# Optimization experiments

Hardware: AMD Instinct MI355X
Metric: run time of the kernel (lower is better)

The kernel has to match this reference:

```python
import jax, jax.numpy as jnp
import numpy as np

B, C, T = 64, 512, 4096
R = 8
H = C // R  # bottleneck = 64


def setup_inputs() -> dict:
    key = jax.random.key(0)
    k1, k2, k3, k4, k5 = jax.random.split(key, 5)
    x = jax.random.normal(k1, (B, C, T), dtype=jnp.float32)
    # PyTorch Linear default init: U(-1/sqrt(fan_in), 1/sqrt(fan_in))
    s1 = 1.0 / np.sqrt(C)
    s2 = 1.0 / np.sqrt(H)
    W1 = jax.random.uniform(k2, (H, C), dtype=jnp.float32, minval=-s1, maxval=s1)
    b1 = jax.random.uniform(k3, (H,), dtype=jnp.float32, minval=-s1, maxval=s1)
    W2 = jax.random.uniform(k4, (C, H), dtype=jnp.float32, minval=-s2, maxval=s2)
    b2 = jax.random.uniform(k5, (C,), dtype=jnp.float32, minval=-s2, maxval=s2)
    return {"x": x, "W1": W1, "b1": b1, "W2": W2, "b2": b2}


def reference(x, W1, b1, W2, b2):
    # squeeze: global average pool over time -> [B, C]
    squeezed = jnp.mean(x, axis=2)
    # excitation: Linear -> ReLU -> Linear -> Sigmoid
    h = jax.nn.relu(squeezed @ W1.T + b1)          # [B, H]
    weights = jax.nn.sigmoid(h @ W2.T + b2)        # [B, C]
    # channel-wise scale
    return x * weights[:, :, None]                 # [B, C, T]
```

## Files before the change

kernel.cpp:

```cpp
#include <hip/hip_runtime.h>
#include <math.h>


#define SE_B 64
#define SE_C 512
#define SE_T 4096
#define SE_H 64

__global__ __launch_bounds__(256) void se_mean(const float* __restrict__ x,
                                               float* __restrict__ sq) {
    const int row = blockIdx.x;
    const float4* __restrict__ xr =
        reinterpret_cast<const float4*>(x + (size_t)row * SE_T);
    float s = 0.f;
    const int t = threadIdx.x;
#pragma unroll
    for (int k = 0; k < 4; ++k) {
        float4 v = xr[t + k * 256];
        s += (v.x + v.y) + (v.z + v.w);
    }
#pragma unroll
    for (int off = 32; off > 0; off >>= 1) s += __shfl_down(s, off, 64);
    __shared__ float wsum[4];
    const int lane = t & 63;
    const int wid = t >> 6;
    if (lane == 0) wsum[wid] = s;
    __syncthreads();
    if (t == 0) {
        float tot = (wsum[0] + wsum[1]) + (wsum[2] + wsum[3]);
        sq[row] = tot * (1.0f / SE_T);
    }
}

__global__ __launch_bounds__(256) void se_mlp(const float* __restrict__ sq,
                                              const float* __restrict__ W1,
                                              const float* __restrict__ b1,
                                              const float* __restrict__ W2,
                                              const float* __restrict__ b2,
                                              float* __restrict__ wt) {
    const int b = blockIdx.x;
    __shared__ float s[SE_C];
    __shared__ float h[SE_H];
    const int t = threadIdx.x;

    for (int c = t; c < SE_C; c += 256) s[c] = sq[b * SE_C + c];
    __syncthreads();

    {
        const int j = t >> 2;
        const int q = t & 3;
        const float* __restrict__ w = W1 + (size_t)j * SE_C;
        float acc = 0.f;
        for (int c = q; c < SE_C; c += 4) acc = fmaf(w[c], s[c], acc);
        acc += __shfl_xor(acc, 1, 64);
        acc += __shfl_xor(acc, 2, 64);
        if (q == 0) h[j] = fmaxf(acc + b1[j], 0.f);
    }
    __syncthreads();

#pragma unroll
    for (int k = 0; k < 2; ++k) {
        const int c = t + k * 256;
        const float* __restrict__ w = W2 + (size_t)c * SE_H;
        float acc = b2[c];
#pragma unroll
        for (int j = 0; j < SE_H; ++j) acc = fmaf(w[j], h[j], acc);
        wt[b * SE_C + c] = 1.0f / (1.0f + expf(-acc));
    }
}

__global__ __launch_bounds__(256) void se_scale(const float* __restrict__ x,
                                                const float* __restrict__ wt,
                                                float* __restrict__ out) {
    const size_t n4 = (size_t)SE_B * SE_C * (SE_T / 4);
    const size_t stride = (size_t)gridDim.x * blockDim.x;
    const float4* __restrict__ x4 = reinterpret_cast<const float4*>(x);
    float4* __restrict__ o4 = reinterpret_cast<float4*>(out);
    for (size_t i = (size_t)blockIdx.x * blockDim.x + threadIdx.x; i < n4;
         i += stride) {
        const int row = (int)(i >> 10);
        const float w = wt[row];
        float4 v = x4[i];
        v.x *= w;
        v.y *= w;
        v.z *= w;
        v.w *= w;
        o4[i] = v;
    }
}

extern "C" void kernel_launch(void* const* d_in, const int* in_sizes, int n_in,
                              void* d_out, int out_size, void* d_ws,
                              size_t ws_size, hipStream_t stream) {
    const float* x = (const float*)d_in[0];
    const float* W1 = (const float*)d_in[1];
    const float* b1 = (const float*)d_in[2];
    const float* W2 = (const float*)d_in[3];
    const float* b2 = (const float*)d_in[4];
    float* out = (float*)d_out;

    float* sq = (float*)d_ws;
    float* wt = sq + SE_B * SE_C;

    se_mean<<<SE_B * SE_C, 256, 0, stream>>>(x, sq);
    se_mlp<<<SE_B, 256, 0, stream>>>(sq, W1, b1, W2, b2, wt);
    se_scale<<<2048, 256, 0, stream>>>(x, wt, out);
}
```

Baseline: 1.000 ms.

## Scale rows in reverse order with nontemporal stores to reuse cached input

The scale kernel now launches one block per row and processes rows in reverse order relative to the mean kernel. Rows read most recently by the mean pass may still be resident in the last-level cache when the scale pass reads them. Output is written with nontemporal stores so it does not evict cached input. The grid-stride loop is replaced by a large fixed grid, which adds block scheduling overhead in exchange for this locality.

```diff
diff --git a/kernel.cpp b/kernel.cpp
--- a/kernel.cpp
+++ b/kernel.cpp
@@ -6,30 +6,29 @@
 #define SE_C 512
 #define SE_T 4096
 #define SE_H 64
+#define SE_ROWS (SE_B * SE_C)
+
+typedef float fv4 __attribute__((ext_vector_type(4)));
 
 __global__ __launch_bounds__(256) void se_mean(const float* __restrict__ x,
                                                float* __restrict__ sq) {
     const int row = blockIdx.x;
-    const float4* __restrict__ xr =
-        reinterpret_cast<const float4*>(x + (size_t)row * SE_T);
-    float s = 0.f;
+    const fv4* __restrict__ xr =
+        reinterpret_cast<const fv4*>(x + (size_t)row * SE_T);
     const int t = threadIdx.x;
-#pragma unroll
-    for (int k = 0; k < 4; ++k) {
-        float4 v = xr[t + k * 256];
-        s += (v.x + v.y) + (v.z + v.w);
-    }
+    fv4 a = xr[t];
+    fv4 b = xr[t + 256];
+    fv4 c = xr[t + 512];
+    fv4 d = xr[t + 768];
+    float s = ((a.x + a.y) + (a.z + a.w)) + ((b.x + b.y) + (b.z + b.w)) +
+              ((c.x + c.y) + (c.z + c.w)) + ((d.x + d.y) + (d.z + d.w));
 #pragma unroll
     for (int off = 32; off > 0; off >>= 1) s += __shfl_down(s, off, 64);
     __shared__ float wsum[4];
-    const int lane = t & 63;
-    const int wid = t >> 6;
-    if (lane == 0) wsum[wid] = s;
+    if ((t & 63) == 0) wsum[t >> 6] = s;
     __syncthreads();
-    if (t == 0) {
-        float tot = (wsum[0] + wsum[1]) + (wsum[2] + wsum[3]);
-        sq[row] = tot * (1.0f / SE_T);
-    }
+    if (t == 0)
+        sq[row] = ((wsum[0] + wsum[1]) + (wsum[2] + wsum[3])) * (1.0f / SE_T);
 }
 
 __global__ __launch_bounds__(256) void se_mlp(const float* __restrict__ sq,
@@ -72,20 +71,17 @@
 __global__ __launch_bounds__(256) void se_scale(const float* __restrict__ x,
                                                 const float* __restrict__ wt,
                                                 float* __restrict__ out) {
-    const size_t n4 = (size_t)SE_B * SE_C * (SE_T / 4);
-    const size_t stride = (size_t)gridDim.x * blockDim.x;
-    const float4* __restrict__ x4 = reinterpret_cast<const float4*>(x);
-    float4* __restrict__ o4 = reinterpret_cast<float4*>(out);
-    for (size_t i = (size_t)blockIdx.x * blockDim.x + threadIdx.x; i < n4;
-         i += stride) {
-        const int row = (int)(i >> 10);
-        const float w = wt[row];
-        float4 v = x4[i];
-        v.x *= w;
-        v.y *= w;
-        v.z *= w;
-        v.w *= w;
-        o4[i] = v;
+    const int row = (SE_ROWS - 1) - (int)blockIdx.x;
+    const float w = wt[row];
+    const fv4* __restrict__ xr =
+        reinterpret_cast<const fv4*>(x + (size_t)row * SE_T);
+    fv4* __restrict__ orow = reinterpret_cast<fv4*>(out + (size_t)row * SE_T);
+    const int t = threadIdx.x;
+#pragma unroll
+    for (int k = 0; k < 4; ++k) {
+        fv4 v = xr[t + k * 256];
+        v *= w;
+        __builtin_nontemporal_store(v, &orow[t + k * 256]);
     }
 }
 
@@ -100,9 +96,9 @@
     float* out = (float*)d_out;
 
     float* sq = (float*)d_ws;
-    float* wt = sq + SE_B * SE_C;
+    float* wt = sq + SE_ROWS;
 
-    se_mean<<<SE_B * SE_C, 256, 0, stream>>>(x, sq);
+    se_mean<<<SE_ROWS, 256, 0, stream>>>(x, sq);
     se_mlp<<<SE_B, 256, 0, stream>>>(sq, W1, b1, W2, b2, wt);
-    se_scale<<<2048, 256, 0, stream>>>(x, wt, out);
+    se_scale<<<SE_ROWS, 256, 0, stream>>>(x, wt, out);
 }
```

After: 937.7 us. 1.07x faster.
